# Kernel tuning notes

Measured on AMD Instinct MI355X. Metric: run time of the kernel, lower is better.

## Reference

```python
import jax, jax.numpy as jnp
import numpy as np

N = 8000      # num_nodes
U = 64        # num_units
D = 2         # input_dim
K = 2         # max_diffusion_step
E = 64000     # edges per support
B = 32        # batch
F = D + U     # concat feature size = 66
M = 2 * K + 1 # num_matrices = 5


def setup_inputs() -> dict:
    key = jax.random.key(0)
    ks = jax.random.split(key, 10)
    return {
        "inputs": jax.random.normal(ks[0], (B, N * D), dtype=jnp.float32),
        "hx": jax.random.normal(ks[1], (B, N * U), dtype=jnp.float32),
        "row0": jax.random.randint(ks[2], (E,), 0, N, dtype=jnp.int32),
        "col0": jax.random.randint(ks[3], (E,), 0, N, dtype=jnp.int32),
        "val0": jax.random.uniform(ks[4], (E,), dtype=jnp.float32) / 8.0,
        "row1": jax.random.randint(ks[5], (E,), 0, N, dtype=jnp.int32),
        "col1": jax.random.randint(ks[6], (E,), 0, N, dtype=jnp.int32),
        "val1": jax.random.uniform(ks[7], (E,), dtype=jnp.float32) / 8.0,
        "W_ru": jax.random.normal(ks[8], (F * M, 2 * U), dtype=jnp.float32) * 0.05,
        "b_ru": jnp.ones((2 * U,), dtype=jnp.float32),  # bias_start=1.0
        "W_c": jax.random.normal(ks[9], (F * M, U), dtype=jnp.float32) * 0.05,
        "b_c": jnp.zeros((U,), dtype=jnp.float32),       # bias_start=0.0
    }


def _spmm(row, col, val, x):
    # y[r] += val_e * x[c]  for each edge e=(r,c); x: [N, F*B]
    return jax.ops.segment_sum(val[:, None] * x[col], row, num_segments=N)


def _gconv(inputs, state, W, b, supports, output_size):
    # inputs: [B, N*D_in], state: [B, N*D_st]
    x = jnp.concatenate([inputs.reshape(B, N, -1), state.reshape(B, N, -1)], axis=2)  # [B,N,F]
    f = x.shape[2]
    x0 = x.transpose(1, 2, 0).reshape(N, f * B)  # [N, F*B]
    xs = [x0]
    for (row, col, val) in supports:
        x1 = _spmm(row, col, val, x0)
        xs.append(x1)
        xk_1, xk_2 = x1, x0
        for _ in range(2, K + 1):
            x2 = 2.0 * _spmm(row, col, val, xk_1) - xk_2
            xs.append(x2)
            xk_1, xk_2 = x2, xk_1
    m = len(xs)
    # [M,N,F,B] -> [B,N,F,M] -> [B*N, F*M]
    xc = jnp.stack(xs).reshape(m, N, f, B).transpose(3, 1, 2, 0).reshape(B * N, f * m)
    out = xc @ W + b
    return out.reshape(B, N * output_size)


def reference(inputs, hx, row0, col0, val0, row1, col1, val1, W_ru, b_ru, W_c, b_c):
    supports = ((row0, col0, val0), (row1, col1, val1))
    # reset/update gates via graph convolution
    value = jax.nn.sigmoid(_gconv(inputs, hx, W_ru, b_ru, supports, 2 * U))
    value = value.reshape(B, N, 2 * U)
    r = value[..., :U].reshape(B, N * U)
    u = value[..., U:].reshape(B, N * U)
    c = jnp.tanh(_gconv(inputs, r * hx, W_c, b_c, supports, U))
    new_state = u * hx + (1.0 - u) * c
    return new_state
```

## Files before the change

### kernel.cpp

```cpp
#include <hip/hip_runtime.h>
#include <stdint.h>

#define NN 8000
#define UU 64
#define EE 64000
#define BB 32
#define NB 256000
#define HXS 512000

typedef __attribute__((ext_vector_type(8))) __bf16 bf16x8;
typedef __attribute__((ext_vector_type(4))) float f32x4;
typedef __attribute__((ext_vector_type(4))) unsigned int u32x4;
typedef __attribute__((ext_vector_type(2))) unsigned int u32x2;

__device__ __forceinline__ unsigned short f2bf(float f){
  unsigned int u = __builtin_bit_cast(unsigned int, f);
  u += 0x7fffu + ((u >> 16) & 1u);
  return (unsigned short)(u >> 16);
}
__device__ __forceinline__ unsigned int pack2(float a, float b){
  return (unsigned int)f2bf(a) | ((unsigned int)f2bf(b) << 16);
}
__device__ __forceinline__ float bflo(unsigned int w){ return __builtin_bit_cast(float, w << 16); }
__device__ __forceinline__ float bfhi(unsigned int w){ return __builtin_bit_cast(float, w & 0xffff0000u); }
__device__ __forceinline__ float bfu(unsigned short v){ return __builtin_bit_cast(float, (unsigned int)v << 16); }

__device__ __forceinline__ void acc8(float* a, float v, uint4 q){
  a[0]+=v*bflo(q.x); a[1]+=v*bfhi(q.x); a[2]+=v*bflo(q.y); a[3]+=v*bfhi(q.y);
  a[4]+=v*bflo(q.z); a[5]+=v*bfhi(q.z); a[6]+=v*bflo(q.w); a[7]+=v*bfhi(q.w);
}

__device__ __forceinline__ void stage16(const unsigned short* g, unsigned short* ldsbase){
  __builtin_amdgcn_global_load_lds((const __attribute__((address_space(1))) void*)g,
                                   (__attribute__((address_space(3))) void*)ldsbase, 16, 0, 0);
}

__device__ __forceinline__ void ntstore16(uint4 v, uint4* p){
  u32x4 ov = {v.x, v.y, v.z, v.w};
  __builtin_nontemporal_store(ov, (u32x4*)p);
}
__device__ __forceinline__ void ntstore8(uint2 v, uint2* p){
  u32x2 ov = {v.x, v.y};
  __builtin_nontemporal_store(ov, (u32x2*)p);
}

__global__ void k_hist(const int* __restrict__ r0, const int* __restrict__ r1, int* __restrict__ cnt){
  int i = blockIdx.x * 256 + threadIdx.x;
  if (i < 2*EE){
    int s = (i >= EE);
    int r = s ? r1[i - EE] : r0[i];
    atomicAdd(&cnt[s*NN + r], 1);
  }
}

__global__ __launch_bounds__(1024) void k_scan(const int* __restrict__ cnt, int* __restrict__ row_ptr, int* __restrict__ rp_work){
  int sup = blockIdx.x;
  const int* c = cnt + sup*NN;
  __shared__ int part[1024];
  int t = threadIdx.x;
  int loc[8]; int s = 0;
  #pragma unroll
  for (int j=0;j<8;j++){ int idx=t*8+j; int v = (idx<NN)? c[idx]:0; loc[j]=s; s+=v; }
  part[t]=s; __syncthreads();
  for (int o=1;o<1024;o<<=1){
    int v = (t>=o)? part[t-o]:0;
    __syncthreads();
    part[t]+=v;
    __syncthreads();
  }
  int pre = (t>0)? part[t-1]:0;
  #pragma unroll
  for (int j=0;j<8;j++){ int idx=t*8+j; if(idx<NN){ int e=pre+loc[j]; row_ptr[sup*(NN+1)+idx]=e; rp_work[sup*NN+idx]=e; } }
  if (t==1023) row_ptr[sup*(NN+1)+NN] = part[1023];
}

__global__ void k_scatter(const int* __restrict__ r0, const int* __restrict__ c0, const float* __restrict__ v0,
                          const int* __restrict__ r1, const int* __restrict__ c1, const float* __restrict__ v1,
                          int* __restrict__ rp_work, uint2* __restrict__ edge_s){
  int i = blockIdx.x * 256 + threadIdx.x;
  if (i < 2*EE){
    int s = (i >= EE);
    int e = s ? i - EE : i;
    int r  = s ? r1[e] : r0[e];
    int cc = s ? c1[e] : c0[e];
    float vv = s ? v1[e] : v0[e];
    int pos = atomicAdd(&rp_work[s*NN + r], 1);
    uint2 ev; ev.x = (unsigned int)cc; ev.y = __builtin_bit_cast(unsigned int, vv);
    edge_s[s*EE + pos] = ev;
  }
}

__global__ void k_wpack(const float* __restrict__ W_ru, const float* __restrict__ W_c,
                        unsigned short* __restrict__ Wru_t, unsigned short* __restrict__ Wc_t){
  int i = blockIdx.x * 256 + threadIdx.x;
  int k = i / 192; int oo = i % 192;
  const float* W; int ld, NC; unsigned short* dst; int c;
  if (oo < 128){ W = W_ru; ld = 128; NC = 128; dst = Wru_t; c = oo; }
  else         { W = W_c;  ld = 64;  NC = 64;  dst = Wc_t;  c = oo - 128; }
  int o = 4*(c & 15) + ((c >> 4) & 3);
  int wcol = (c >= 64) ? 64 + o : o;
  float v = 0.f;
  if (k < 330){
    int m, fb;
    if (k < 320){ m = k >> 6; fb = (2 + (k & 63)) * 5; }
    else        { int j = k - 320; m = j >> 1; fb = (j & 1) * 5; }
    if      (m==0) v = W[(fb+0)*ld+wcol] - W[(fb+2)*ld+wcol] - W[(fb+4)*ld+wcol];
    else if (m==1) v = W[(fb+1)*ld+wcol];
    else if (m==2) v = 2.f*W[(fb+2)*ld+wcol];
    else if (m==3) v = W[(fb+3)*ld+wcol];
    else           v = 2.f*W[(fb+4)*ld+wcol];
  }
  int dstoff;
  if (k < 320) dstoff = (k>>6)*NC*64 + c*64 + (k&63);
  else         dstoff = 320*NC + c*32 + (k-320);
  dst[dstoff] = f2bf(v);
}

__global__ void k_x0(const float* __restrict__ inputs, const float* __restrict__ hx,
                     uint4* __restrict__ xs0q, unsigned int* __restrict__ xi0){
  int n = blockIdx.x, t = threadIdx.x;
  int b = t >> 3, ug = t & 7;
  const float4 h0 = *(const float4*)(hx + (size_t)b*HXS + n*64 + ug*8);
  const float4 h1 = *(const float4*)(hx + (size_t)b*HXS + n*64 + ug*8 + 4);
  uint4 o;
  o.x = pack2(h0.x, h0.y); o.y = pack2(h0.z, h0.w);
  o.z = pack2(h1.x, h1.y); o.w = pack2(h1.z, h1.w);
  xs0q[((size_t)n*32 + b)*8 + ug] = o;
  if (t < 32){
    int bb = t;
    const float2 g = *(const float2*)(inputs + (size_t)bb*(NN*2) + n*2);
    xi0[(((size_t)(bb>>2)*NN) + n)*4 + (bb&3)] = pack2(g.x, g.y);
  }
}

template<int NSUP, bool WITH_IN>
__global__ __launch_bounds__(256) void k_spmm(const int* __restrict__ row_ptr, const uint2* __restrict__ edge_s,
                                              unsigned short* xsS, uint4* xi4,
                                              int supE0, int msrc0, int mdst0,
                                              int supE1, int msrc1, int mdst1){
  constexpr int NSTATE = NSUP*16000;
  int bid = blockIdx.x;
  if (WITH_IN && bid >= NSTATE){
    int b2 = bid - NSTATE;
    int s = b2 & 7;
    int si = (NSUP == 2) ? ((b2 >> 3) & 1) : 0;
    int chunk = (NSUP == 2) ? (b2 >> 4) : (b2 >> 3);
    int n = chunk*256 + threadIdx.x;
    if (n >= NN) return;
    int supE = si ? supE1 : supE0;
    int msrc = si ? msrc1 : msrc0;
    int mdst = si ? mdst1 : mdst0;
    size_t sb = (size_t)(msrc*8 + s)*NN, db = (size_t)(mdst*8 + s)*NN;
    int beg = row_ptr[supE*(NN+1)+n], end = row_ptr[supE*(NN+1)+n+1];
    const uint2* es = edge_s + supE*EE;
    float ai[8] = {0.f,0.f,0.f,0.f,0.f,0.f,0.f,0.f};
    for (int e = beg; e < end; ++e){
      uint2 ev = es[e];
      float v = __builtin_bit_cast(float, ev.y);
      uint4 qi = xi4[sb + ev.x];
      acc8(ai, v, qi);
    }
    uint4 oi;
    oi.x = pack2(ai[0],ai[1]); oi.y = pack2(ai[2],ai[3]); oi.z = pack2(ai[4],ai[5]); oi.w = pack2(ai[6],ai[7]);
    ntstore16(oi, &xi4[db + n]);
    return;
  }
  int g = __builtin_amdgcn_readfirstlane(bid*4 + (threadIdx.x >> 6));
  int slice, si, n;
  if (NSUP == 2){
    slice = g / 16000; int r = g - slice*16000;
    si = (r >= 8000) ? 1 : 0; n = r - si*8000;
  } else {
    slice = g / 8000; si = 0; n = g - slice*8000;
  }
  int supE = si ? supE1 : supE0;
  int msrc = si ? msrc1 : msrc0;
  int mdst = si ? mdst1 : mdst0;
  int lane = threadIdx.x & 63;
  int off = slice*256 + lane*4;
  const unsigned short* srcS = xsS + (size_t)msrc*(NN*2048);
  unsigned short* dstS = xsS + (size_t)mdst*(NN*2048);
  int beg = __builtin_amdgcn_readfirstlane(row_ptr[supE*(NN+1)+n]);
  int end = __builtin_amdgcn_readfirstlane(row_ptr[supE*(NN+1)+n+1]);
  const uint2* es = edge_s + supE*EE;

  float a0=0.f, a1=0.f, a2=0.f, a3=0.f;
  int e = beg;
  for (; e + 2 <= end; e += 2){
    uint2 ev0 = es[e], ev1 = es[e+1];
    int c0 = __builtin_amdgcn_readfirstlane((int)ev0.x);
    int c1 = __builtin_amdgcn_readfirstlane((int)ev1.x);
    float v0 = __builtin_bit_cast(float, __builtin_amdgcn_readfirstlane(ev0.y));
    float v1 = __builtin_bit_cast(float, __builtin_amdgcn_readfirstlane(ev1.y));
    const unsigned short* rp0 = srcS + (size_t)c0*2048;
    const unsigned short* rp1 = srcS + (size_t)c1*2048;
    uint2 q0 = *(const uint2*)(rp0 + off);
    uint2 q1 = *(const uint2*)(rp1 + off);
    a0 += v0*bflo(q0.x); a1 += v0*bfhi(q0.x); a2 += v0*bflo(q0.y); a3 += v0*bfhi(q0.y);
    a0 += v1*bflo(q1.x); a1 += v1*bfhi(q1.x); a2 += v1*bflo(q1.y); a3 += v1*bfhi(q1.y);
  }
  if (e < end){
    uint2 ev = es[e];
    int c = __builtin_amdgcn_readfirstlane((int)ev.x);
    float v = __builtin_bit_cast(float, __builtin_amdgcn_readfirstlane(ev.y));
    const unsigned short* rp = srcS + (size_t)c*2048;
    uint2 q = *(const uint2*)(rp + off);
    a0 += v*bflo(q.x); a1 += v*bfhi(q.x); a2 += v*bflo(q.y); a3 += v*bfhi(q.y);
  }
  uint2 o; o.x = pack2(a0, a1); o.y = pack2(a2, a3);
  ntstore8(o, (uint2*)(dstS + (size_t)n*2048 + off));
}

template<int NCOL, bool IS_RU>
__global__ __launch_bounds__(256, 3) void k_gemm(unsigned short* xsS,
                                                 const unsigned int* __restrict__ xsI,
                                                 const unsigned short* __restrict__ Wp,
                                                 const float* __restrict__ bias,
                                                 const float* __restrict__ hx,
                                                 float* cout,
                                                 unsigned short* ubuf){
  constexpr int CF = NCOL / 16;
  __shared__ unsigned short Bl[2][NCOL*64];
  __shared__ unsigned short Bt[NCOL*32];
  const int t = threadIdx.x;
  const int wv = t >> 6;
  const int l = t & 63;
  const int lr = l & 15;
  const int lg = l >> 4;
  const int R0 = blockIdx.x * 128;

  auto stageB = [&](int m, int buf){
    #pragma unroll
    for (int i=0;i<NCOL*8/256;i++){
      int g = t + i*256;
      int rr = g >> 3, c = g & 7;
      const unsigned short* gp = Wp + (size_t)(m*NCOL + rr)*64 + ((c ^ (rr&7)) << 3);
      stage16(gp, &Bl[buf][(size_t)(i*256 + wv*64)*8]);
    }
  };

  size_t abase[2];
  #pragma unroll
  for (int rf=0; rf<2; rf++)
    abase[rf] = (size_t)(R0 + wv*32 + rf*16 + lr)*64;
  auto loadA = [&](int m, uint4* dst){
    #pragma unroll
    for (int ks=0; ks<2; ks++)
      #pragma unroll
      for (int rf=0; rf<2; rf++)
        dst[ks*2+rf] = *(const uint4*)(xsS + (size_t)m*(NN*2048) + abase[rf] + ks*32 + lg*8);
  };

  uint4 aC[4], aN[4];
  loadA(0, aC);
  uint4 aT[2];
  #pragma unroll
  for (int rf=0; rf<2; rf++){
    int row = R0 + wv*32 + rf*16 + lr;
    int n = row >> 5, b = row & 31;
    size_t ib = (((size_t)(b>>2))*NN + n)*4 + (b&3);
    unsigned int q0=0u,q1=0u,q2=0u,q3=0u;
    if (lg == 0){
      q0 = xsI[ib];
      q1 = xsI[(size_t)8*NN*4 + ib];
      q2 = xsI[(size_t)16*NN*4 + ib];
      q3 = xsI[(size_t)24*NN*4 + ib];
    } else if (lg == 1){
      q0 = xsI[(size_t)32*NN*4 + ib];
    }
    uint4 qq; qq.x=q0; qq.y=q1; qq.z=q2; qq.w=q3;
    aT[rf] = qq;
  }
  stageB(0, 0);
  {
    #pragma unroll
    for (int i=0;i<NCOL*4/256;i++){
      int g = t + i*256;
      int rr = g >> 2, c = g & 3;
      const unsigned short* gp = Wp + (size_t)320*NCOL + rr*32 + ((c ^ (rr&3)) << 3);
      stage16(gp, &Bt[(size_t)(i*256 + wv*64)*8]);
    }
  }
  __syncthreads();

  f32x4 acc[2][CF];
  const f32x4 zero = {0.f,0.f,0.f,0.f};
  #pragma unroll
  for (int rf=0; rf<2; rf++)
    #pragma unroll
    for (int cf=0; cf<CF; cf++) acc[rf][cf] = zero;

  #pragma unroll
  for (int m=0; m<5; m++){
    int cur = m & 1;
    if (m < 4){
      stageB(m+1, cur^1);
      loadA(m+1, aN);
    }
    #pragma unroll
    for (int ks=0; ks<2; ks++){
      #pragma unroll
      for (int cf=0; cf<CF; cf++){
        int col = cf*16 + lr;
        int chunk = (ks*4 + lg) ^ (col & 7);
        bf16x8 bv = __builtin_bit_cast(bf16x8, *(const uint4*)(&Bl[cur][col*64 + chunk*8]));
        acc[0][cf] = __builtin_amdgcn_mfma_f32_16x16x32_bf16(__builtin_bit_cast(bf16x8, aC[ks*2+0]), bv, acc[0][cf], 0, 0, 0);
        acc[1][cf] = __builtin_amdgcn_mfma_f32_16x16x32_bf16(__builtin_bit_cast(bf16x8, aC[ks*2+1]), bv, acc[1][cf], 0, 0, 0);
      }
    }
    __syncthreads();
    #pragma unroll
    for (int i=0;i<4;i++) aC[i] = aN[i];
  }

  #pragma unroll
  for (int cf=0; cf<CF; cf++){
    int col = cf*16 + lr;
    int chunk = lg ^ (col & 3);
    bf16x8 bv = __builtin_bit_cast(bf16x8, *(const uint4*)(&Bt[col*32 + chunk*8]));
    acc[0][cf] = __builtin_amdgcn_mfma_f32_16x16x32_bf16(__builtin_bit_cast(bf16x8, aT[0]), bv, acc[0][cf], 0, 0, 0);
    acc[1][cf] = __builtin_amdgcn_mfma_f32_16x16x32_bf16(__builtin_bit_cast(bf16x8, aT[1]), bv, acc[1][cf], 0, 0, 0);
  }

  #pragma unroll
  for (int rf=0; rf<2; rf++){
    #pragma unroll
    for (int reg=0; reg<4; reg++){
      int row = R0 + wv*32 + rf*16 + (lg << 2) + reg;
      int n = row >> 5, b = row & 31;
      size_t rowoff = (size_t)b*HXS + (size_t)n*UU;
      size_t slot0 = (size_t)row*64;
      int o0 = lr << 2;
      if constexpr (IS_RU){
        uint2 hv = *(const uint2*)(xsS + slot0 + o0);
        unsigned short rr4[4], uu4[4];
        #pragma unroll
        for (int cf=0; cf<4; cf++){
          int o = o0 + cf;
          float vr = acc[rf][cf][reg]   + bias[o];
          float vu = acc[rf][cf+4][reg] + bias[64+o];
          float sgr = 1.f/(1.f + __expf(-vr));
          float sgu = 1.f/(1.f + __expf(-vu));
          float h = bfu(((const unsigned short*)&hv)[cf]);
          rr4[cf] = f2bf(sgr * h);
          uu4[cf] = f2bf(sgu);
        }
        *(uint2*)(xsS + slot0 + o0) = *(uint2*)rr4;
        *(uint2*)(ubuf + rowoff + o0) = *(uint2*)uu4;
      } else {
        float4 hv = *(const float4*)(hx + rowoff + o0);
        uint2 uv = *(const uint2*)(ubuf + rowoff + o0);
        float4 ov;
        #pragma unroll
        for (int cf=0; cf<4; cf++){
          float cc = tanhf(acc[rf][cf][reg] + bias[o0+cf]);
          float uu = bfu(((const unsigned short*)&uv)[cf]);
          float h  = ((const float*)&hv)[cf];
          ((float*)&ov)[cf] = uu*h + (1.f - uu)*cc;
        }
        *(float4*)(cout + rowoff + o0) = ov;
      }
    }
  }
}

extern "C" void kernel_launch(void* const* d_in, const int* in_sizes, int n_in,
                              void* d_out, int out_size, void* d_ws, size_t ws_size,
                              hipStream_t stream){
  const float* inputs = (const float*)d_in[0];
  const float* hx     = (const float*)d_in[1];
  const int*   row0   = (const int*)d_in[2];
  const int*   col0   = (const int*)d_in[3];
  const float* val0   = (const float*)d_in[4];
  const int*   row1   = (const int*)d_in[5];
  const int*   col1   = (const int*)d_in[6];
  const float* val1   = (const float*)d_in[7];
  const float* W_ru   = (const float*)d_in[8];
  const float* b_ru   = (const float*)d_in[9];
  const float* W_c    = (const float*)d_in[10];
  const float* b_c    = (const float*)d_in[11];
  float* out = (float*)d_out;

  char* ws = (char*)d_ws;
  size_t off = 0;
  auto alloc = [&](size_t bytes) -> void* {
    void* p = ws + off;
    off += (bytes + 255) & ~(size_t)255;
    return p;
  };
  unsigned short* xsS   = (unsigned short*)alloc((size_t)5*NN*2048*2);
  unsigned int*   xsI   = (unsigned int*)  alloc((size_t)5*8*NN*16);
  unsigned short* u_buf = (unsigned short*)alloc((size_t)NB*64*2);
  unsigned short* Wru_t = (unsigned short*)alloc((size_t)128*352*2);
  unsigned short* Wc_t  = (unsigned short*)alloc((size_t)64*352*2);
  int*   row_ptr = (int*)  alloc(2*(NN+1)*4);
  uint2* edge_s  = (uint2*)alloc((size_t)2*EE*8);
  int*   cnt     = (int*)  alloc(2*NN*4);
  int*   rp_work = (int*)  alloc(2*NN*4);
  (void)ws_size; (void)in_sizes; (void)n_in; (void)out_size;

  hipMemsetAsync(cnt, 0, 2*NN*4, stream);
  k_hist<<<(2*EE + 255)/256, 256, 0, stream>>>(row0, row1, cnt);
  k_scan<<<2, 1024, 0, stream>>>(cnt, row_ptr, rp_work);
  k_scatter<<<(2*EE + 255)/256, 256, 0, stream>>>(row0, col0, val0, row1, col1, val1, rp_work, edge_s);
  k_wpack<<<(352*192)/256, 256, 0, stream>>>(W_ru, W_c, Wru_t, Wc_t);
  k_x0<<<NN, 256, 0, stream>>>(inputs, hx, (uint4*)xsS, (unsigned int*)xsI);

  uint4* xi4 = (uint4*)xsI;

  k_spmm<2, true ><<<32512, 256, 0, stream>>>(row_ptr, edge_s, xsS, xi4, 0, 0, 1, 1, 0, 3);
  k_spmm<1, true ><<<16256, 256, 0, stream>>>(row_ptr, edge_s, xsS, xi4, 0, 1, 2, 0, 1, 2);
  k_spmm<1, true ><<<16256, 256, 0, stream>>>(row_ptr, edge_s, xsS, xi4, 1, 3, 4, 1, 3, 4);
  k_gemm<128, true><<<2000, 256, 0, stream>>>(xsS, xsI, Wru_t, b_ru, hx, nullptr, u_buf);

  k_spmm<2, false><<<32000, 256, 0, stream>>>(row_ptr, edge_s, xsS, xi4, 0, 0, 1, 1, 0, 3);
  k_spmm<1, false><<<16000, 256, 0, stream>>>(row_ptr, edge_s, xsS, xi4, 0, 1, 2, 0, 1, 2);
  k_spmm<1, false><<<16000, 256, 0, stream>>>(row_ptr, edge_s, xsS, xi4, 1, 3, 4, 1, 3, 4);
  k_gemm<64, false><<<2000, 256, 0, stream>>>(xsS, xsI, Wc_t, b_c, hx, out, u_buf);
}
```

Measured before the change: 451.2 us.

## Merge second-hop SpMM of both supports into one launch and raise gemm occupancy

```diff
diff --git a/kernel.cpp b/kernel.cpp
--- a/kernel.cpp
+++ b/kernel.cpp
@@ -133,18 +133,15 @@
   }
 }
 
-template<int NSUP, bool WITH_IN>
+template<bool WITH_IN>
 __global__ __launch_bounds__(256) void k_spmm(const int* __restrict__ row_ptr, const uint2* __restrict__ edge_s,
                                               unsigned short* xsS, uint4* xi4,
                                               int supE0, int msrc0, int mdst0,
                                               int supE1, int msrc1, int mdst1){
-  constexpr int NSTATE = NSUP*16000;
   int bid = blockIdx.x;
-  if (WITH_IN && bid >= NSTATE){
-    int b2 = bid - NSTATE;
-    int s = b2 & 7;
-    int si = (NSUP == 2) ? ((b2 >> 3) & 1) : 0;
-    int chunk = (NSUP == 2) ? (b2 >> 4) : (b2 >> 3);
+  if (WITH_IN && bid >= 32000){
+    int b2 = bid - 32000;
+    int s = b2 & 7, si = (b2 >> 3) & 1, chunk = b2 >> 4;
     int n = chunk*256 + threadIdx.x;
     if (n >= NN) return;
     int supE = si ? supE1 : supE0;
@@ -166,13 +163,10 @@
     return;
   }
   int g = __builtin_amdgcn_readfirstlane(bid*4 + (threadIdx.x >> 6));
-  int slice, si, n;
-  if (NSUP == 2){
-    slice = g / 16000; int r = g - slice*16000;
-    si = (r >= 8000) ? 1 : 0; n = r - si*8000;
-  } else {
-    slice = g / 8000; si = 0; n = g - slice*8000;
-  }
+  int w = g / 8000;
+  int n = g - w*8000;
+  int slice = w >> 1;
+  int si = w & 1;
   int supE = si ? supE1 : supE0;
   int msrc = si ? msrc1 : msrc0;
   int mdst = si ? mdst1 : mdst0;
@@ -212,7 +206,7 @@
 }
 
 template<int NCOL, bool IS_RU>
-__global__ __launch_bounds__(256, 3) void k_gemm(unsigned short* xsS,
+__global__ __launch_bounds__(256, IS_RU ? 4 : 6) void k_gemm(unsigned short* xsS,
                                                  const unsigned int* __restrict__ xsI,
                                                  const unsigned short* __restrict__ Wp,
                                                  const float* __restrict__ bias,
@@ -408,13 +402,11 @@
 
   uint4* xi4 = (uint4*)xsI;
 
-  k_spmm<2, true ><<<32512, 256, 0, stream>>>(row_ptr, edge_s, xsS, xi4, 0, 0, 1, 1, 0, 3);
-  k_spmm<1, true ><<<16256, 256, 0, stream>>>(row_ptr, edge_s, xsS, xi4, 0, 1, 2, 0, 1, 2);
-  k_spmm<1, true ><<<16256, 256, 0, stream>>>(row_ptr, edge_s, xsS, xi4, 1, 3, 4, 1, 3, 4);
+  k_spmm<true ><<<32512, 256, 0, stream>>>(row_ptr, edge_s, xsS, xi4, 0, 0, 1, 1, 0, 3);
+  k_spmm<true ><<<32512, 256, 0, stream>>>(row_ptr, edge_s, xsS, xi4, 0, 1, 2, 1, 3, 4);
   k_gemm<128, true><<<2000, 256, 0, stream>>>(xsS, xsI, Wru_t, b_ru, hx, nullptr, u_buf);
 
-  k_spmm<2, false><<<32000, 256, 0, stream>>>(row_ptr, edge_s, xsS, xi4, 0, 0, 1, 1, 0, 3);
-  k_spmm<1, false><<<16000, 256, 0, stream>>>(row_ptr, edge_s, xsS, xi4, 0, 1, 2, 0, 1, 2);
-  k_spmm<1, false><<<16000, 256, 0, stream>>>(row_ptr, edge_s, xsS, xi4, 1, 3, 4, 1, 3, 4);
+  k_spmm<false><<<32000, 256, 0, stream>>>(row_ptr, edge_s, xsS, xi4, 0, 0, 1, 1, 0, 3);
+  k_spmm<false><<<32000, 256, 0, stream>>>(row_ptr, edge_s, xsS, xi4, 0, 1, 2, 1, 3, 4);
   k_gemm<64, false><<<2000, 256, 0, stream>>>(xsS, xsI, Wc_t, b_c, hx, out, u_buf);
 }
```

Measured after the change: 461.3 us. 1.02x slower.
